# Performance work log

Hardware: AMD Instinct MI355X
Metric: run time of the kernel (lower is better)

Reference implementation:

```python
import jax, jax.numpy as jnp
import numpy as np

EPS = 1e-12

def sage_layer(x, src, dst, Wl, Wr, b, n_nodes):
    # mean aggregation of source-node features into destination nodes
    msgs = x[src]                                            # [E, F] gather
    s = jax.ops.segment_sum(msgs, dst, num_segments=n_nodes)  # [N, F]
    cnt = jax.ops.segment_sum(jnp.ones((src.shape[0],), x.dtype), dst, num_segments=n_nodes)
    agg = s / jnp.maximum(cnt, 1.0)[:, None]                 # mean; 0 for isolated nodes
    out = agg @ Wl + b + x @ Wr                              # lin_l(agg) + lin_r(x_i)
    norm = jnp.linalg.norm(out, axis=-1, keepdims=True)      # normalize=True -> L2 norm
    return out / jnp.maximum(norm, EPS)


def setup_inputs() -> dict:
    key = jax.random.key(0)
    ks = jax.random.split(key, 8)
    N, E, F = 100000, 1200000, 64
    H1, H2, OUT = 64, 32, 10  # hidden_channels//2, hidden_channels//4, output_dim
    x = jax.random.normal(ks[0], (N, F), dtype=jnp.float32)
    edge_index = jax.random.randint(ks[1], (2, E), 0, N, dtype=jnp.int64)
    def glorot(k, fin, fout):
        lim = np.sqrt(6.0 / (fin + fout)).astype(np.float32)
        return jax.random.uniform(k, (fin, fout), jnp.float32, -lim, lim)
    return {
        "x": x,
        "edge_index": edge_index,
        "W1l": glorot(ks[2], F, H1), "W1r": glorot(ks[3], F, H1), "b1": jnp.zeros((H1,), jnp.float32),
        "W2l": glorot(ks[4], H1, H2), "W2r": glorot(ks[5], H1, H2), "b2": jnp.zeros((H2,), jnp.float32),
        "W3l": glorot(ks[6], H2, OUT), "W3r": glorot(ks[7], H2, OUT), "b3": jnp.zeros((OUT,), jnp.float32),
    }


def reference(x, edge_index, W1l, W1r, b1, W2l, W2r, b2, W3l, W3r, b3):
    n = x.shape[0]
    src, dst = edge_index[0], edge_index[1]
    h = jax.nn.relu(sage_layer(x, src, dst, W1l, W1r, b1, n))
    h = jax.nn.relu(sage_layer(h, src, dst, W2l, W2r, b2, n))
    h = sage_layer(h, src, dst, W3l, W3r, b3, n)
    return jax.nn.log_softmax(h, axis=1)
```

## Files before the change

### kernel.cpp

```cpp
#include <hip/hip_runtime.h>
#include <math.h>


typedef __attribute__((ext_vector_type(8))) short short8;
typedef __attribute__((ext_vector_type(4))) float floatx4;
typedef __attribute__((ext_vector_type(2))) float floatx2;

__device__ __forceinline__ unsigned short f2bf(float f) {
    unsigned u = __float_as_uint(f);
    u += 0x7fffu + ((u >> 16) & 1u);
    return (unsigned short)(u >> 16);
}
__device__ __forceinline__ float blo(unsigned u) { return __uint_as_float(u << 16); }
__device__ __forceinline__ float bhi(unsigned u) { return __uint_as_float(u & 0xffff0000u); }
__device__ __forceinline__ unsigned char f2fp8(float f) {
    return (unsigned char)(__builtin_amdgcn_cvt_pk_fp8_f32(f, f, 0, false) & 0xFF);
}


__global__ __launch_bounds__(256) void hist_kernel(
        const int* __restrict__ ei, int* __restrict__ bh, int* __restrict__ sync_ctr,
        int E, int NB, int NBKT) {
    __shared__ int lh[256];
    const int tid = threadIdx.x, blk = blockIdx.x;
    if (blk == 0 && tid == 0) *sync_ctr = 0;
    lh[tid] = 0;
    __syncthreads();
    const int base = blk << 12;
#pragma unroll
    for (int i = 0; i < 16; ++i) {
        const int e = base + (i << 8) + tid;
        if (e < E) atomicAdd(&lh[min((int)(((unsigned)ei[E + e]) >> 9), NBKT - 1)], 1);
    }
    __syncthreads();
    if (tid < NBKT) bh[tid * NB + blk] = lh[tid];
}

__global__ __launch_bounds__(256) void bscan_kernel(
        const int* __restrict__ bh, int* __restrict__ offs, int* __restrict__ btot,
        int* __restrict__ bucket_base, int* __restrict__ sync_ctr,
        int NB, int NBKT) {
    const int lane = threadIdx.x & 63;
    const int w = blockIdx.x * 4 + (threadIdx.x >> 6);
    if (w < NBKT) {
        int running = 0;
        for (int base = 0; base < NB; base += 64) {
            const int j = base + lane;
            const int v = (j < NB) ? bh[w * NB + j] : 0;
            int incl = v;
#pragma unroll
            for (int off = 1; off < 64; off <<= 1) {
                const int t = __shfl_up(incl, off);
                if (lane >= off) incl += t;
            }
            if (j < NB) offs[w * NB + j] = running + incl - v;
            running += __shfl(incl, 63);
        }
        if (lane == 0) btot[w] = running;
    }
    __threadfence();
    __syncthreads();
    __shared__ int amLast;
    if (threadIdx.x == 0) amLast = (atomicAdd(sync_ctr, 1) == (int)gridDim.x - 1);
    __syncthreads();
    if (amLast && threadIdx.x < 64) {
        __threadfence();
        int running = 0;
        for (int base = 0; base < NBKT; base += 64) {
            const int j = base + threadIdx.x;
            const int v = (j < NBKT) ? btot[j] : 0;
            int incl = v;
#pragma unroll
            for (int off = 1; off < 64; off <<= 1) {
                const int t = __shfl_up(incl, off);
                if ((int)threadIdx.x >= off) incl += t;
            }
            if (j < NBKT) bucket_base[j] = running + incl - v;
            running += __shfl(incl, 63);
        }
        if (threadIdx.x == 0) bucket_base[NBKT] = running;
    }
}

template <int K, int F_OUT, int PAD, bool AFP32, bool YL8>
__global__ __launch_bounds__(256) void scatter_t1_kernel(
        const int* __restrict__ ei, const int* __restrict__ offs,
        const int* __restrict__ bucket_base, unsigned* __restrict__ ebuf,
        int E, int NB, int NBKT,
        const void* __restrict__ Ain, const float* __restrict__ Wl,
        const float* __restrict__ Wr, const float* __restrict__ b,
        void* __restrict__ yl, unsigned short* __restrict__ yr, int n) {
    __shared__ int lcur[256];
    const int tid = threadIdx.x;
    if ((int)blockIdx.x < NB) {
        const int blk = blockIdx.x;
        if (tid < NBKT) lcur[tid] = bucket_base[tid] + offs[tid * NB + blk];
        __syncthreads();
        const int base = blk << 12;
#pragma unroll
        for (int i = 0; i < 16; ++i) {
            const int e = base + (i << 8) + tid;
            if (e < E) {
                const int s = ei[e];
                const unsigned d = (unsigned)ei[E + e];
                int p = atomicAdd(&lcur[min((int)(d >> 9), NBKT - 1)], 1);
                p = min(p, E - 1);
                ebuf[p] = ((d & 511u) << 17) | (unsigned)s;
            }
        }
        return;
    }
    constexpr int KSTEP = K / 32;
    constexpr int NT = PAD / 16;
    const int lane = tid & 63;
    const int wid = (((int)blockIdx.x - NB) * 256 + tid) >> 6;
    const int ntiles = (n + 15) >> 4;
    if (wid >= ntiles) return;
    const int nl = lane & 15, q = lane >> 4;

    short8 Bl[NT][KSTEP], Br[NT][KSTEP];
    float biasv[NT];
#pragma unroll
    for (int t = 0; t < NT; ++t) {
        const int ncol = t * 16 + nl;
        biasv[t] = (ncol < F_OUT) ? b[ncol] : 0.f;
#pragma unroll
        for (int ks = 0; ks < KSTEP; ++ks) {
#pragma unroll
            for (int j = 0; j < 8; ++j) {
                const int k = ks * 32 + q * 8 + j;
                Bl[t][ks][j] = (ncol < F_OUT) ? (short)f2bf(Wl[k * F_OUT + ncol]) : (short)0;
                Br[t][ks][j] = (ncol < F_OUT) ? (short)f2bf(Wr[k * F_OUT + ncol]) : (short)0;
            }
        }
    }

    const int m0 = wid * 16;
    int m = m0 + nl; if (m >= n) m = n - 1;

    short8 a[KSTEP];
#pragma unroll
    for (int ks = 0; ks < KSTEP; ++ks) {
        if (AFP32) {
            const float* p = (const float*)Ain + (size_t)m * K + ks * 32 + q * 8;
#pragma unroll
            for (int j = 0; j < 8; ++j) a[ks][j] = (short)f2bf(p[j]);
        } else {
            union { uint4 u; short8 s; } cvt;
            cvt.u = *(const uint4*)((const unsigned short*)Ain + (size_t)m * K + ks * 32 + q * 8);
            a[ks] = cvt.s;
        }
    }

    floatx4 accl[NT], accr[NT];
#pragma unroll
    for (int t = 0; t < NT; ++t) { accl[t] = {0.f,0.f,0.f,0.f}; accr[t] = {0.f,0.f,0.f,0.f}; }
#pragma unroll
    for (int ks = 0; ks < KSTEP; ++ks) {
#pragma unroll
        for (int t = 0; t < NT; ++t) {
            accl[t] = __builtin_amdgcn_mfma_f32_16x16x32_bf16(a[ks], Bl[t][ks], accl[t], 0, 0, 0);
            accr[t] = __builtin_amdgcn_mfma_f32_16x16x32_bf16(a[ks], Br[t][ks], accr[t], 0, 0, 0);
        }
    }

#pragma unroll
    for (int t = 0; t < NT; ++t) {
        const int ncol = t * 16 + nl;
#pragma unroll
        for (int r = 0; r < 4; ++r) {
            const int node = m0 + q * 4 + r;
            if (node < n) {
                if (YL8)
                    ((unsigned char*)yl)[(size_t)node * PAD + ncol] = f2fp8(accl[t][r]);
                else
                    ((unsigned short*)yl)[(size_t)node * PAD + ncol] = f2bf(accl[t][r]);
                yr[(size_t)node * PAD + ncol] = f2bf(accr[t][r] + biasv[t]);
            }
        }
    }
}

__global__ __launch_bounds__(512) void bucket_csr_kernel(
        const unsigned* __restrict__ ebuf, const int* __restrict__ bucket_base,
        int* __restrict__ rowptr, int* __restrict__ deg, int* __restrict__ col,
        int N, int E) {
    __shared__ unsigned long long lcnt[512];
    __shared__ int lcur[2048];
    __shared__ int wsum[8];
    const int b = blockIdx.x, tid = threadIdx.x;
    const int q1 = N >> 2, q2 = N >> 1, q3 = (N >> 2) + (N >> 1);
    const int segbase = bucket_base[b];
    const int L = bucket_base[b + 1] - segbase;
    lcnt[tid] = 0ull;
    __syncthreads();
    for (int i = tid; i < L; i += 512) {
        const unsigned p = ebuf[segbase + i];
        const int ln = p >> 17;
        const int s  = (int)(p & 0x1FFFFu);
        const int q  = (s < q2) ? ((s < q1) ? 0 : 1) : ((s < q3) ? 2 : 3);
        atomicAdd(&lcnt[ln], 1ull << (q << 4));
    }
    __syncthreads();
    const unsigned long long cv = lcnt[tid];
    const int f0 = (int)(cv & 0xFFFFu),         f1 = (int)((cv >> 16) & 0xFFFFu);
    const int f2 = (int)((cv >> 32) & 0xFFFFu), f3 = (int)((cv >> 48) & 0xFFFFu);
    const int dnode = f0 + f1 + f2 + f3;
    const int lane = tid & 63, w = tid >> 6;
    int incl = dnode;
#pragma unroll
    for (int off = 1; off < 64; off <<= 1) {
        const int t = __shfl_up(incl, off);
        if (lane >= off) incl += t;
    }
    if (lane == 63) wsum[w] = incl;
    __syncthreads();
    int wbase = 0;
#pragma unroll
    for (int ww = 0; ww < 8; ++ww) if (ww < w) wbase += wsum[ww];
    const int excl = wbase + incl - dnode;
    const int node = (b << 9) + tid;
    if (node < N) { rowptr[node] = segbase + excl; deg[node] = dnode; }
    lcur[tid]        = excl;
    lcur[512 + tid]  = excl + f0;
    lcur[1024 + tid] = excl + f0 + f1;
    lcur[1536 + tid] = excl + f0 + f1 + f2;
    __syncthreads();
    for (int i = tid; i < L; i += 512) {
        const unsigned p = ebuf[segbase + i];
        const int ln = p >> 17;
        const int s  = (int)(p & 0x1FFFFu);
        const int q  = (s < q2) ? ((s < q1) ? 0 : 1) : ((s < q3) ? 2 : 3);
        int pos = atomicAdd(&lcur[(q << 9) + ln], 1);
        pos = min(segbase + pos, E - 1);
        col[pos] = s;
    }
}

template <int K, int F_OUT, int PAD, bool AFP32, bool YL8>
__global__ __launch_bounds__(256) void transform_kernel(
        const void* __restrict__ Ain, const float* __restrict__ Wl,
        const float* __restrict__ Wr, const float* __restrict__ b,
        void* __restrict__ yl, unsigned short* __restrict__ yr, int n) {
    constexpr int KSTEP = K / 32;
    constexpr int NT = PAD / 16;
    const int lane = threadIdx.x & 63;
    const int wid = (blockIdx.x * blockDim.x + threadIdx.x) >> 6;
    const int ntiles = (n + 15) >> 4;
    if (wid >= ntiles) return;
    const int nl = lane & 15, q = lane >> 4;

    short8 Bl[NT][KSTEP], Br[NT][KSTEP];
    float biasv[NT];
#pragma unroll
    for (int t = 0; t < NT; ++t) {
        const int ncol = t * 16 + nl;
        biasv[t] = (ncol < F_OUT) ? b[ncol] : 0.f;
#pragma unroll
        for (int ks = 0; ks < KSTEP; ++ks) {
#pragma unroll
            for (int j = 0; j < 8; ++j) {
                const int k = ks * 32 + q * 8 + j;
                Bl[t][ks][j] = (ncol < F_OUT) ? (short)f2bf(Wl[k * F_OUT + ncol]) : (short)0;
                Br[t][ks][j] = (ncol < F_OUT) ? (short)f2bf(Wr[k * F_OUT + ncol]) : (short)0;
            }
        }
    }

    const int m0 = wid * 16;
    int m = m0 + nl; if (m >= n) m = n - 1;

    short8 a[KSTEP];
#pragma unroll
    for (int ks = 0; ks < KSTEP; ++ks) {
        if (AFP32) {
            const float* p = (const float*)Ain + (size_t)m * K + ks * 32 + q * 8;
#pragma unroll
            for (int j = 0; j < 8; ++j) a[ks][j] = (short)f2bf(p[j]);
        } else {
            union { uint4 u; short8 s; } cvt;
            cvt.u = *(const uint4*)((const unsigned short*)Ain + (size_t)m * K + ks * 32 + q * 8);
            a[ks] = cvt.s;
        }
    }

    floatx4 accl[NT], accr[NT];
#pragma unroll
    for (int t = 0; t < NT; ++t) { accl[t] = {0.f,0.f,0.f,0.f}; accr[t] = {0.f,0.f,0.f,0.f}; }
#pragma unroll
    for (int ks = 0; ks < KSTEP; ++ks) {
#pragma unroll
        for (int t = 0; t < NT; ++t) {
            accl[t] = __builtin_amdgcn_mfma_f32_16x16x32_bf16(a[ks], Bl[t][ks], accl[t], 0, 0, 0);
            accr[t] = __builtin_amdgcn_mfma_f32_16x16x32_bf16(a[ks], Br[t][ks], accr[t], 0, 0, 0);
        }
    }

#pragma unroll
    for (int t = 0; t < NT; ++t) {
        const int ncol = t * 16 + nl;
#pragma unroll
        for (int r = 0; r < 4; ++r) {
            const int node = m0 + q * 4 + r;
            if (node < n) {
                if (YL8)
                    ((unsigned char*)yl)[(size_t)node * PAD + ncol] = f2fp8(accl[t][r]);
                else
                    ((unsigned short*)yl)[(size_t)node * PAD + ncol] = f2bf(accl[t][r]);
                yr[(size_t)node * PAD + ncol] = f2bf(accr[t][r] + biasv[t]);
            }
        }
    }
}

template <int F, int ACT, int PK>
__global__ __launch_bounds__(256) void agg_kernel(
        const void* __restrict__ yl, const unsigned short* __restrict__ yr,
        const int* __restrict__ rowptr, const int* __restrict__ degv,
        const int* __restrict__ col,
        unsigned short* __restrict__ hout, float* __restrict__ fout, int n) {
    constexpr int G = F / 8;
    constexpr int NPW = 64 / G;
    const int lane = threadIdx.x & 63;
    const int wid = (blockIdx.x * blockDim.x + threadIdx.x) >> 6;
    const int g = lane / G, c = lane % G;
    const int node = wid * NPW + g;
    if (node >= n) return;

    const int beg = rowptr[node];
    const int dg  = degv[node];
    const int nmax = n - 1;

    float a0=0.f,a1=0.f,a2=0.f,a3=0.f,a4=0.f,a5=0.f,a6=0.f,a7=0.f;
    int i = 0;
    if (PK == 1) {
        const unsigned char* base = (const unsigned char*)yl + c * 8;
        auto accrow = [&](uint2 t) {
            const floatx2 p0 = __builtin_amdgcn_cvt_pk_f32_fp8((int)t.x, false);
            const floatx2 p1 = __builtin_amdgcn_cvt_pk_f32_fp8((int)t.x, true);
            const floatx2 p2 = __builtin_amdgcn_cvt_pk_f32_fp8((int)t.y, false);
            const floatx2 p3 = __builtin_amdgcn_cvt_pk_f32_fp8((int)t.y, true);
            a0 += p0.x; a1 += p0.y; a2 += p1.x; a3 += p1.y;
            a4 += p2.x; a5 += p2.y; a6 += p3.x; a7 += p3.y;
        };
        if (dg >= 4) {
            int c0 = col[beg], c1 = col[beg+1], c2 = col[beg+2], c3 = col[beg+3];
            for (; i + 8 <= dg; i += 4) {
                const int d0 = col[beg+i+4], d1 = col[beg+i+5];
                const int d2 = col[beg+i+6], d3 = col[beg+i+7];
                const uint2 t0 = *(const uint2*)(base + (size_t)min(c0,nmax) * F);
                const uint2 t1 = *(const uint2*)(base + (size_t)min(c1,nmax) * F);
                const uint2 t2 = *(const uint2*)(base + (size_t)min(c2,nmax) * F);
                const uint2 t3 = *(const uint2*)(base + (size_t)min(c3,nmax) * F);
                accrow(t0); accrow(t1); accrow(t2); accrow(t3);
                c0 = d0; c1 = d1; c2 = d2; c3 = d3;
            }
            const uint2 t0 = *(const uint2*)(base + (size_t)min(c0,nmax) * F);
            const uint2 t1 = *(const uint2*)(base + (size_t)min(c1,nmax) * F);
            const uint2 t2 = *(const uint2*)(base + (size_t)min(c2,nmax) * F);
            const uint2 t3 = *(const uint2*)(base + (size_t)min(c3,nmax) * F);
            accrow(t0); accrow(t1); accrow(t2); accrow(t3);
            i += 4;
        }
        for (; i < dg; ++i)
            accrow(*(const uint2*)(base + (size_t)min(col[beg+i],nmax) * F));
    } else {
        const unsigned short* base = (const unsigned short*)yl + c * 8;
        auto accrow4 = [&](uint4 t) {
            a0 += blo(t.x); a1 += bhi(t.x); a2 += blo(t.y); a3 += bhi(t.y);
            a4 += blo(t.z); a5 += bhi(t.z); a6 += blo(t.w); a7 += bhi(t.w);
        };
        if (dg >= 4) {
            int c0 = col[beg], c1 = col[beg+1], c2 = col[beg+2], c3 = col[beg+3];
            for (; i + 8 <= dg; i += 4) {
                const int d0 = col[beg+i+4], d1 = col[beg+i+5];
                const int d2 = col[beg+i+6], d3 = col[beg+i+7];
                const uint4 t0 = *(const uint4*)(base + (size_t)min(c0,nmax) * F);
                const uint4 t1 = *(const uint4*)(base + (size_t)min(c1,nmax) * F);
                const uint4 t2 = *(const uint4*)(base + (size_t)min(c2,nmax) * F);
                const uint4 t3 = *(const uint4*)(base + (size_t)min(c3,nmax) * F);
                accrow4(t0); accrow4(t1); accrow4(t2); accrow4(t3);
                c0 = d0; c1 = d1; c2 = d2; c3 = d3;
            }
            const uint4 t0 = *(const uint4*)(base + (size_t)min(c0,nmax) * F);
            const uint4 t1 = *(const uint4*)(base + (size_t)min(c1,nmax) * F);
            const uint4 t2 = *(const uint4*)(base + (size_t)min(c2,nmax) * F);
            const uint4 t3 = *(const uint4*)(base + (size_t)min(c3,nmax) * F);
            accrow4(t0); accrow4(t1); accrow4(t2); accrow4(t3);
            i += 4;
        }
        for (; i < dg; ++i)
            accrow4(*(const uint4*)(base + (size_t)min(col[beg+i],nmax) * F));
    }
    const float inv = (dg > 0) ? 1.f / (float)dg : 0.f;

    const uint4 rv = *(const uint4*)(yr + (size_t)node * F + c * 8);
    float o[8];
    o[0] = a0*inv + blo(rv.x); o[1] = a1*inv + bhi(rv.x);
    o[2] = a2*inv + blo(rv.y); o[3] = a3*inv + bhi(rv.y);
    o[4] = a4*inv + blo(rv.z); o[5] = a5*inv + bhi(rv.z);
    o[6] = a6*inv + blo(rv.w); o[7] = a7*inv + bhi(rv.w);

    float ss = 0.f;
#pragma unroll
    for (int j = 0; j < 8; ++j) ss += o[j] * o[j];
#pragma unroll
    for (int off = 1; off < G; off <<= 1) ss += __shfl_xor(ss, off);
    const float scale = 1.f / fmaxf(sqrtf(ss), 1e-12f);

    if (ACT == 1) {
        uint4 u;
        float h[8];
#pragma unroll
        for (int j = 0; j < 8; ++j) h[j] = fmaxf(o[j] * scale, 0.f);
        u.x = (unsigned)f2bf(h[0]) | ((unsigned)f2bf(h[1]) << 16);
        u.y = (unsigned)f2bf(h[2]) | ((unsigned)f2bf(h[3]) << 16);
        u.z = (unsigned)f2bf(h[4]) | ((unsigned)f2bf(h[5]) << 16);
        u.w = (unsigned)f2bf(h[6]) | ((unsigned)f2bf(h[7]) << 16);
        *(uint4*)(hout + (size_t)node * F + c * 8) = u;
    } else {
#pragma unroll
        for (int j = 0; j < 8; ++j) o[j] *= scale;
        const int cbase = c * 8;
        float m = -INFINITY;
#pragma unroll
        for (int j = 0; j < 8; ++j) if (cbase + j < 10) m = fmaxf(m, o[j]);
        m = fmaxf(m, __shfl_xor(m, 1));
        float s = 0.f;
#pragma unroll
        for (int j = 0; j < 8; ++j) if (cbase + j < 10) s += __expf(o[j] - m);
        s += __shfl_xor(s, 1);
        const float ls = logf(s);
#pragma unroll
        for (int j = 0; j < 8; ++j)
            if (cbase + j < 10) fout[(size_t)node * 10 + cbase + j] = o[j] - m - ls;
    }
}

extern "C" void kernel_launch(void* const* d_in, const int* in_sizes, int n_in,
                              void* d_out, int out_size, void* d_ws, size_t ws_size,
                              hipStream_t stream) {
    const float* x   = (const float*)d_in[0];
    const int*   ei  = (const int*)d_in[1];
    const float* W1l = (const float*)d_in[2];
    const float* W1r = (const float*)d_in[3];
    const float* b1  = (const float*)d_in[4];
    const float* W2l = (const float*)d_in[5];
    const float* W2r = (const float*)d_in[6];
    const float* b2  = (const float*)d_in[7];
    const float* W3l = (const float*)d_in[8];
    const float* W3r = (const float*)d_in[9];
    const float* b3  = (const float*)d_in[10];
    float*       out = (float*)d_out;

    const int N = in_sizes[0] / 64;
    const int E = in_sizes[1] / 2;
    const int NBKT = (N + 511) >> 9;
    const int NB   = (E + 4095) >> 12;

    auto align16 = [](size_t v) { return (v + 15) & ~(size_t)15; };
    char* ws = (char*)d_ws;
    size_t off = 0;
    int* rowptr  = (int*)(ws + off); off = align16(off + (size_t)N * 4);
    int* deg     = (int*)(ws + off); off = align16(off + (size_t)N * 4);
    int* colidx  = (int*)(ws + off); off = align16(off + (size_t)E * 4);
    unsigned* ebuf = (unsigned*)(ws + off); off = align16(off + (size_t)E * 4);
    int* bh      = (int*)(ws + off); off = align16(off + (size_t)NBKT * NB * 4);
    int* offsb   = (int*)(ws + off); off = align16(off + (size_t)NBKT * NB * 4);
    int* btot    = (int*)(ws + off); off = align16(off + (size_t)NBKT * 4);
    int* bbase   = (int*)(ws + off); off = align16(off + (size_t)(NBKT + 1) * 4);
    int* sctr    = (int*)(ws + off); off = align16(off + 16);
    unsigned char*  y1l = (unsigned char*)(ws + off);  off = align16(off + (size_t)N * 64);
    unsigned short* y1r = (unsigned short*)(ws + off); off = align16(off + (size_t)N * 64 * 2);
    unsigned short* h1  = (unsigned short*)(ws + off); off = align16(off + (size_t)N * 64 * 2);
    unsigned char*  y2l = (unsigned char*)(ws + off);  off = align16(off + (size_t)N * 32);
    unsigned short* y2r = (unsigned short*)(ws + off); off = align16(off + (size_t)N * 32 * 2);
    unsigned short* h2  = (unsigned short*)(ws + off); off = align16(off + (size_t)N * 32 * 2);
    unsigned short* y3l = (unsigned short*)(ws + off); off = align16(off + (size_t)N * 16 * 2);
    unsigned short* y3r = (unsigned short*)(ws + off); off = align16(off + (size_t)N * 16 * 2);
    (void)ws_size; (void)n_in; (void)out_size;

    const int ntiles = (N + 15) / 16;
    const int tblocks = (ntiles * 64 + 255) / 256;

    hist_kernel<<<NB, 256, 0, stream>>>(ei, bh, sctr, E, NB, NBKT);
    bscan_kernel<<<(NBKT + 3) / 4, 256, 0, stream>>>(bh, offsb, btot, bbase, sctr, NB, NBKT);
    scatter_t1_kernel<64, 64, 64, true, true><<<NB + tblocks, 256, 0, stream>>>(
        ei, offsb, bbase, ebuf, E, NB, NBKT,
        x, W1l, W1r, b1, y1l, y1r, N);
    bucket_csr_kernel<<<NBKT, 512, 0, stream>>>(ebuf, bbase, rowptr, deg, colidx, N, E);

    agg_kernel<64, 1, 1><<<(N + 31) / 32, 256, 0, stream>>>(
        y1l, y1r, rowptr, deg, colidx, h1, nullptr, N);
    transform_kernel<64, 32, 32, false, true><<<tblocks, 256, 0, stream>>>(
        h1, W2l, W2r, b2, y2l, y2r, N);
    agg_kernel<32, 1, 1><<<(N + 63) / 64, 256, 0, stream>>>(
        y2l, y2r, rowptr, deg, colidx, h2, nullptr, N);
    transform_kernel<32, 10, 16, false, false><<<tblocks, 256, 0, stream>>>(
        h2, W3l, W3r, b3, y3l, y3r, N);
    agg_kernel<16, 2, 0><<<(N + 127) / 128, 256, 0, stream>>>(
        y3l, y3r, rowptr, deg, colidx, nullptr, out, N);
}
```

Measured before the change: 206.7 us.

## Fuse mean aggregation with next layer's MFMA transform via LDS tiles

Replaces the separate agg and transform kernels for layers 1 and 2 with a fused kernel. Each wave aggregates 16 nodes, normalizes them, applies ReLU and writes them as bf16 into shared memory, then runs the next layer's MFMA projections directly from LDS. This removes the h1/h2 global round-trips and two kernel launches. In exchange each wave gathers its 16 nodes over several serial rounds, which may reduce memory-level parallelism in the gather phase.

```diff
diff --git a/kernel.cpp b/kernel.cpp
--- a/kernel.cpp
+++ b/kernel.cpp
@@ -237,52 +237,121 @@
     }
 }
 
-template <int K, int F_OUT, int PAD, bool AFP32, bool YL8>
-__global__ __launch_bounds__(256) void transform_kernel(
-        const void* __restrict__ Ain, const float* __restrict__ Wl,
-        const float* __restrict__ Wr, const float* __restrict__ b,
-        void* __restrict__ yl, unsigned short* __restrict__ yr, int n) {
-    constexpr int KSTEP = K / 32;
-    constexpr int NT = PAD / 16;
-    const int lane = threadIdx.x & 63;
-    const int wid = (blockIdx.x * blockDim.x + threadIdx.x) >> 6;
+template <int F, int FO, int PADO, bool YL8O>
+__global__ __launch_bounds__(256) void aggt_kernel(
+        const unsigned char* __restrict__ yl, const unsigned short* __restrict__ yr,
+        const int* __restrict__ rowptr, const int* __restrict__ degv,
+        const int* __restrict__ col,
+        const float* __restrict__ Wl, const float* __restrict__ Wr,
+        const float* __restrict__ bia,
+        void* __restrict__ ylo, unsigned short* __restrict__ yro, int n) {
+    constexpr int G = F / 8;
+    constexpr int NPW = 64 / G;
+    constexpr int ROUNDS = 16 / NPW;
+    constexpr int S = F + 8;
+    constexpr int KSTEP = F / 32;
+    constexpr int NT = PADO / 16;
+    __shared__ __align__(16) unsigned short hloc[4][16][S];
+    const int tid = threadIdx.x;
+    const int lane = tid & 63;
+    const int wv = tid >> 6;
+    const int wid = (blockIdx.x * 256 + tid) >> 6;
     const int ntiles = (n + 15) >> 4;
     if (wid >= ntiles) return;
+    const int g = lane / G, c = lane % G;
     const int nl = lane & 15, q = lane >> 4;
+    const int nmax = n - 1;
 
     short8 Bl[NT][KSTEP], Br[NT][KSTEP];
     float biasv[NT];
 #pragma unroll
     for (int t = 0; t < NT; ++t) {
         const int ncol = t * 16 + nl;
-        biasv[t] = (ncol < F_OUT) ? b[ncol] : 0.f;
+        biasv[t] = (ncol < FO) ? bia[ncol] : 0.f;
 #pragma unroll
         for (int ks = 0; ks < KSTEP; ++ks) {
 #pragma unroll
             for (int j = 0; j < 8; ++j) {
                 const int k = ks * 32 + q * 8 + j;
-                Bl[t][ks][j] = (ncol < F_OUT) ? (short)f2bf(Wl[k * F_OUT + ncol]) : (short)0;
-                Br[t][ks][j] = (ncol < F_OUT) ? (short)f2bf(Wr[k * F_OUT + ncol]) : (short)0;
-            }
-        }
-    }
-
-    const int m0 = wid * 16;
-    int m = m0 + nl; if (m >= n) m = n - 1;
+                Bl[t][ks][j] = (ncol < FO) ? (short)f2bf(Wl[k * FO + ncol]) : (short)0;
+                Br[t][ks][j] = (ncol < FO) ? (short)f2bf(Wr[k * FO + ncol]) : (short)0;
+            }
+        }
+    }
+
+    const int tbase = wid * 16;
+#pragma unroll
+    for (int r = 0; r < ROUNDS; ++r) {
+        const int nrow = r * NPW + g;
+        const int node = min(tbase + nrow, nmax);
+        const int beg = rowptr[node];
+        const int dg  = degv[node];
+
+        float a0=0.f,a1=0.f,a2=0.f,a3=0.f,a4=0.f,a5=0.f,a6=0.f,a7=0.f;
+        {
+            const unsigned char* base = yl + c * 8;
+            auto accrow = [&](uint2 t) {
+                const floatx2 p0 = __builtin_amdgcn_cvt_pk_f32_fp8((int)t.x, false);
+                const floatx2 p1 = __builtin_amdgcn_cvt_pk_f32_fp8((int)t.x, true);
+                const floatx2 p2 = __builtin_amdgcn_cvt_pk_f32_fp8((int)t.y, false);
+                const floatx2 p3 = __builtin_amdgcn_cvt_pk_f32_fp8((int)t.y, true);
+                a0 += p0.x; a1 += p0.y; a2 += p1.x; a3 += p1.y;
+                a4 += p2.x; a5 += p2.y; a6 += p3.x; a7 += p3.y;
+            };
+            int i = 0;
+            if (dg >= 4) {
+                int c0 = col[beg], c1 = col[beg+1], c2 = col[beg+2], c3 = col[beg+3];
+                for (; i + 8 <= dg; i += 4) {
+                    const int d0 = col[beg+i+4], d1 = col[beg+i+5];
+                    const int d2 = col[beg+i+6], d3 = col[beg+i+7];
+                    const uint2 t0 = *(const uint2*)(base + (size_t)min(c0,nmax) * F);
+                    const uint2 t1 = *(const uint2*)(base + (size_t)min(c1,nmax) * F);
+                    const uint2 t2 = *(const uint2*)(base + (size_t)min(c2,nmax) * F);
+                    const uint2 t3 = *(const uint2*)(base + (size_t)min(c3,nmax) * F);
+                    accrow(t0); accrow(t1); accrow(t2); accrow(t3);
+                    c0 = d0; c1 = d1; c2 = d2; c3 = d3;
+                }
+                const uint2 t0 = *(const uint2*)(base + (size_t)min(c0,nmax) * F);
+                const uint2 t1 = *(const uint2*)(base + (size_t)min(c1,nmax) * F);
+                const uint2 t2 = *(const uint2*)(base + (size_t)min(c2,nmax) * F);
+                const uint2 t3 = *(const uint2*)(base + (size_t)min(c3,nmax) * F);
+                accrow(t0); accrow(t1); accrow(t2); accrow(t3);
+                i += 4;
+            }
+            for (; i < dg; ++i)
+                accrow(*(const uint2*)(base + (size_t)min(col[beg+i],nmax) * F));
+        }
+        const float inv = (dg > 0) ? 1.f / (float)dg : 0.f;
+
+        const uint4 rv = *(const uint4*)(yr + (size_t)node * F + c * 8);
+        float o[8];
+        o[0] = a0*inv + blo(rv.x); o[1] = a1*inv + bhi(rv.x);
+        o[2] = a2*inv + blo(rv.y); o[3] = a3*inv + bhi(rv.y);
+        o[4] = a4*inv + blo(rv.z); o[5] = a5*inv + bhi(rv.z);
+        o[6] = a6*inv + blo(rv.w); o[7] = a7*inv + bhi(rv.w);
+
+        float ss = 0.f;
+#pragma unroll
+        for (int j = 0; j < 8; ++j) ss += o[j] * o[j];
+#pragma unroll
+        for (int off = 1; off < G; off <<= 1) ss += __shfl_xor(ss, off);
+        const float scale = 1.f / fmaxf(sqrtf(ss), 1e-12f);
+
+        uint4 u;
+        float h[8];
+#pragma unroll
+        for (int j = 0; j < 8; ++j) h[j] = fmaxf(o[j] * scale, 0.f);
+        u.x = (unsigned)f2bf(h[0]) | ((unsigned)f2bf(h[1]) << 16);
+        u.y = (unsigned)f2bf(h[2]) | ((unsigned)f2bf(h[3]) << 16);
+        u.z = (unsigned)f2bf(h[4]) | ((unsigned)f2bf(h[5]) << 16);
+        u.w = (unsigned)f2bf(h[6]) | ((unsigned)f2bf(h[7]) << 16);
+        *(uint4*)&hloc[wv][nrow][c * 8] = u;
+    }
 
     short8 a[KSTEP];
 #pragma unroll
-    for (int ks = 0; ks < KSTEP; ++ks) {
-        if (AFP32) {
-            const float* p = (const float*)Ain + (size_t)m * K + ks * 32 + q * 8;
-#pragma unroll
-            for (int j = 0; j < 8; ++j) a[ks][j] = (short)f2bf(p[j]);
-        } else {
-            union { uint4 u; short8 s; } cvt;
-            cvt.u = *(const uint4*)((const unsigned short*)Ain + (size_t)m * K + ks * 32 + q * 8);
-            a[ks] = cvt.s;
-        }
-    }
+    for (int ks = 0; ks < KSTEP; ++ks)
+        a[ks] = *(const short8*)&hloc[wv][nl][ks * 32 + q * 8];
 
     floatx4 accl[NT], accr[NT];
 #pragma unroll
@@ -300,14 +369,14 @@
     for (int t = 0; t < NT; ++t) {
         const int ncol = t * 16 + nl;
 #pragma unroll
-        for (int r = 0; r < 4; ++r) {
-            const int node = m0 + q * 4 + r;
+        for (int rr = 0; rr < 4; ++rr) {
+            const int node = tbase + q * 4 + rr;
             if (node < n) {
-                if (YL8)
-                    ((unsigned char*)yl)[(size_t)node * PAD + ncol] = f2fp8(accl[t][r]);
+                if (YL8O)
+                    ((unsigned char*)ylo)[(size_t)node * PADO + ncol] = f2fp8(accl[t][rr]);
                 else
-                    ((unsigned short*)yl)[(size_t)node * PAD + ncol] = f2bf(accl[t][r]);
-                yr[(size_t)node * PAD + ncol] = f2bf(accr[t][r] + biasv[t]);
+                    ((unsigned short*)ylo)[(size_t)node * PADO + ncol] = f2bf(accl[t][rr]);
+                yro[(size_t)node * PADO + ncol] = f2bf(accr[t][rr] + biasv[t]);
             }
         }
     }
@@ -333,38 +402,7 @@
 
     float a0=0.f,a1=0.f,a2=0.f,a3=0.f,a4=0.f,a5=0.f,a6=0.f,a7=0.f;
     int i = 0;
-    if (PK == 1) {
-        const unsigned char* base = (const unsigned char*)yl + c * 8;
-        auto accrow = [&](uint2 t) {
-            const floatx2 p0 = __builtin_amdgcn_cvt_pk_f32_fp8((int)t.x, false);
-            const floatx2 p1 = __builtin_amdgcn_cvt_pk_f32_fp8((int)t.x, true);
-            const floatx2 p2 = __builtin_amdgcn_cvt_pk_f32_fp8((int)t.y, false);
-            const floatx2 p3 = __builtin_amdgcn_cvt_pk_f32_fp8((int)t.y, true);
-            a0 += p0.x; a1 += p0.y; a2 += p1.x; a3 += p1.y;
-            a4 += p2.x; a5 += p2.y; a6 += p3.x; a7 += p3.y;
-        };
-        if (dg >= 4) {
-            int c0 = col[beg], c1 = col[beg+1], c2 = col[beg+2], c3 = col[beg+3];
-            for (; i + 8 <= dg; i += 4) {
-                const int d0 = col[beg+i+4], d1 = col[beg+i+5];
-                const int d2 = col[beg+i+6], d3 = col[beg+i+7];
-                const uint2 t0 = *(const uint2*)(base + (size_t)min(c0,nmax) * F);
-                const uint2 t1 = *(const uint2*)(base + (size_t)min(c1,nmax) * F);
-                const uint2 t2 = *(const uint2*)(base + (size_t)min(c2,nmax) * F);
-                const uint2 t3 = *(const uint2*)(base + (size_t)min(c3,nmax) * F);
-                accrow(t0); accrow(t1); accrow(t2); accrow(t3);
-                c0 = d0; c1 = d1; c2 = d2; c3 = d3;
-            }
-            const uint2 t0 = *(const uint2*)(base + (size_t)min(c0,nmax) * F);
-            const uint2 t1 = *(const uint2*)(base + (size_t)min(c1,nmax) * F);
-            const uint2 t2 = *(const uint2*)(base + (size_t)min(c2,nmax) * F);
-            const uint2 t3 = *(const uint2*)(base + (size_t)min(c3,nmax) * F);
-            accrow(t0); accrow(t1); accrow(t2); accrow(t3);
-            i += 4;
-        }
-        for (; i < dg; ++i)
-            accrow(*(const uint2*)(base + (size_t)min(col[beg+i],nmax) * F));
-    } else {
+    {
         const unsigned short* base = (const unsigned short*)yl + c * 8;
         auto accrow4 = [&](uint4 t) {
             a0 += blo(t.x); a1 += bhi(t.x); a2 += blo(t.y); a3 += bhi(t.y);
@@ -408,33 +446,22 @@
     for (int off = 1; off < G; off <<= 1) ss += __shfl_xor(ss, off);
     const float scale = 1.f / fmaxf(sqrtf(ss), 1e-12f);
 
-    if (ACT == 1) {
-        uint4 u;
-        float h[8];
-#pragma unroll
-        for (int j = 0; j < 8; ++j) h[j] = fmaxf(o[j] * scale, 0.f);
-        u.x = (unsigned)f2bf(h[0]) | ((unsigned)f2bf(h[1]) << 16);
-        u.y = (unsigned)f2bf(h[2]) | ((unsigned)f2bf(h[3]) << 16);
-        u.z = (unsigned)f2bf(h[4]) | ((unsigned)f2bf(h[5]) << 16);
-        u.w = (unsigned)f2bf(h[6]) | ((unsigned)f2bf(h[7]) << 16);
-        *(uint4*)(hout + (size_t)node * F + c * 8) = u;
-    } else {
-#pragma unroll
-        for (int j = 0; j < 8; ++j) o[j] *= scale;
-        const int cbase = c * 8;
-        float m = -INFINITY;
-#pragma unroll
-        for (int j = 0; j < 8; ++j) if (cbase + j < 10) m = fmaxf(m, o[j]);
-        m = fmaxf(m, __shfl_xor(m, 1));
-        float s = 0.f;
-#pragma unroll
-        for (int j = 0; j < 8; ++j) if (cbase + j < 10) s += __expf(o[j] - m);
-        s += __shfl_xor(s, 1);
-        const float ls = logf(s);
-#pragma unroll
-        for (int j = 0; j < 8; ++j)
-            if (cbase + j < 10) fout[(size_t)node * 10 + cbase + j] = o[j] - m - ls;
-    }
+#pragma unroll
+    for (int j = 0; j < 8; ++j) o[j] *= scale;
+    const int cbase = c * 8;
+    float m = -INFINITY;
+#pragma unroll
+    for (int j = 0; j < 8; ++j) if (cbase + j < 10) m = fmaxf(m, o[j]);
+    m = fmaxf(m, __shfl_xor(m, 1));
+    float s = 0.f;
+#pragma unroll
+    for (int j = 0; j < 8; ++j) if (cbase + j < 10) s += __expf(o[j] - m);
+    s += __shfl_xor(s, 1);
+    const float ls = logf(s);
+#pragma unroll
+    for (int j = 0; j < 8; ++j)
+        if (cbase + j < 10) fout[(size_t)node * 10 + cbase + j] = o[j] - m - ls;
+    (void)hout;
 }
 
 extern "C" void kernel_launch(void* const* d_in, const int* in_sizes, int n_in,
@@ -472,16 +499,15 @@
     int* sctr    = (int*)(ws + off); off = align16(off + 16);
     unsigned char*  y1l = (unsigned char*)(ws + off);  off = align16(off + (size_t)N * 64);
     unsigned short* y1r = (unsigned short*)(ws + off); off = align16(off + (size_t)N * 64 * 2);
-    unsigned short* h1  = (unsigned short*)(ws + off); off = align16(off + (size_t)N * 64 * 2);
     unsigned char*  y2l = (unsigned char*)(ws + off);  off = align16(off + (size_t)N * 32);
     unsigned short* y2r = (unsigned short*)(ws + off); off = align16(off + (size_t)N * 32 * 2);
-    unsigned short* h2  = (unsigned short*)(ws + off); off = align16(off + (size_t)N * 32 * 2);
     unsigned short* y3l = (unsigned short*)(ws + off); off = align16(off + (size_t)N * 16 * 2);
     unsigned short* y3r = (unsigned short*)(ws + off); off = align16(off + (size_t)N * 16 * 2);
     (void)ws_size; (void)n_in; (void)out_size;
 
     const int ntiles = (N + 15) / 16;
     const int tblocks = (ntiles * 64 + 255) / 256;
+    const int atblocks = (ntiles + 3) / 4;
 
     hist_kernel<<<NB, 256, 0, stream>>>(ei, bh, sctr, E, NB, NBKT);
     bscan_kernel<<<(NBKT + 3) / 4, 256, 0, stream>>>(bh, offsb, btot, bbase, sctr, NB, NBKT);
@@ -490,14 +516,10 @@
         x, W1l, W1r, b1, y1l, y1r, N);
     bucket_csr_kernel<<<NBKT, 512, 0, stream>>>(ebuf, bbase, rowptr, deg, colidx, N, E);
 
-    agg_kernel<64, 1, 1><<<(N + 31) / 32, 256, 0, stream>>>(
-        y1l, y1r, rowptr, deg, colidx, h1, nullptr, N);
-    transform_kernel<64, 32, 32, false, true><<<tblocks, 256, 0, stream>>>(
-        h1, W2l, W2r, b2, y2l, y2r, N);
-    agg_kernel<32, 1, 1><<<(N + 63) / 64, 256, 0, stream>>>(
-        y2l, y2r, rowptr, deg, colidx, h2, nullptr, N);
-    transform_kernel<32, 10, 16, false, false><<<tblocks, 256, 0, stream>>>(
-        h2, W3l, W3r, b3, y3l, y3r, N);
+    aggt_kernel<64, 32, 32, true><<<atblocks, 256, 0, stream>>>(
+        y1l, y1r, rowptr, deg, colidx, W2l, W2r, b2, y2l, y2r, N);
+    aggt_kernel<32, 10, 16, false><<<atblocks, 256, 0, stream>>>(
+        y2l, y2r, rowptr, deg, colidx, W3l, W3r, b3, y3l, y3r, N);
     agg_kernel<16, 2, 0><<<(N + 127) / 128, 256, 0, stream>>>(
         y3l, y3r, rowptr, deg, colidx, nullptr, out, N);
 }
```

Result: slower. 213.3 us (+3.2%).
